# Kernel optimization log

Hardware: AMD Instinct MI355X
Metric: run time of the kernel (lower is better)

## Reference

```python
import jax, jax.numpy as jnp
import numpy as np

ALPHA, BETA, GAMMA = 1.0, 0.5, 0.1
IGNORE = 255


def setup_inputs() -> dict:
    key = jax.random.key(0)
    k1, k2, k3 = jax.random.split(key, 3)
    n, c, h, w, d = 8, 21, 512, 512, 32
    logit = jax.random.normal(k1, (n, c, h, w), dtype=jnp.float32)
    target = jax.random.randint(k2, (n, 1, h, w), 0, 21, dtype=jnp.int32)
    features_in = jax.random.normal(k3, (n, h * w, d), dtype=jnp.float32)
    return {"logit": logit, "target": target, "features_in": features_in}


def reference(logit, target, features_in):
    n, c, h, w = logit.shape
    P = h * w  # total_size per image (sum of all label counts incl. ignore)
    lab = target.reshape(n, P)
    valid = lab != IGNORE
    lab_safe = jnp.where(valid, lab, 0)
    vm = valid.astype(logit.dtype)

    # --- CE loss (mean over non-ignored pixels, as torch CrossEntropyLoss) ---
    logp = jax.nn.log_softmax(logit, axis=1).transpose(0, 2, 3, 1).reshape(n, P, c)
    ce_pix = -jnp.take_along_axis(logp, lab_safe[..., None], axis=2)[..., 0]
    CE = jnp.sum(ce_pix * vm) / jnp.maximum(jnp.sum(vm), 1.0)

    # --- per-pixel logit terms (VAR / Inter), vectorized over the python loop ---
    logit_f = logit.transpose(0, 2, 3, 1).reshape(n, P, c)  # [n,P,c]
    lg = jnp.take_along_axis(logit_f, lab_safe[..., None], axis=2)[..., 0]  # logit at own label
    VAR = jnp.sum(-lg * vm) / P
    Inter = jnp.sum((jnp.sum(logit_f, axis=-1) - lg) * vm) / P

    # --- Center loss: per-image per-class variance of features_in (segment reduce) ---
    onehot = jax.nn.one_hot(lab_safe, c, dtype=logit.dtype) * vm[..., None]  # [n,P,c]
    counts = jnp.sum(onehot, axis=1)                                    # [n,c]
    sums = jnp.einsum('npc,npd->ncd', onehot, features_in)              # class sums
    sumsq = jnp.einsum('npc,np->nc', onehot, jnp.sum(features_in ** 2, axis=-1))
    # sum ||f - mean||^2 = sum||f||^2 - ||sum f||^2 / count
    mean_term = jnp.sum(sums ** 2, axis=-1) / jnp.maximum(counts, 1.0)
    Center = jnp.sum(jnp.where(counts > 0, sumsq - mean_term, 0.0)) / P

    loss = (CE + ALPHA * VAR + BETA * Inter + GAMMA * Center) / n
    return loss
```

## Files before the change

### kernel.cpp

```cpp
#include <hip/hip_runtime.h>


constexpr int   N_IMG  = 8;
constexpr int   C_CLS  = 21;
constexpr int   P_PIX  = 512 * 512;
constexpr int   PQ     = P_PIX / 4;
constexpr int   IGN    = 255;
constexpr float ALPHA  = 1.0f, BETA = 0.5f, GAMMA = 0.1f;

constexpr int MAIN_BLOCKS = 1024;
constexpr int FEAT_ITERS  = 64;

constexpr int OFF_PIX  = 0;
constexpr int OFF_SSQ  = OFF_PIX + MAIN_BLOCKS * 4;
constexpr int OFF_CLS  = OFF_SSQ + MAIN_BLOCKS;
constexpr int OFF_CNT  = OFF_CLS + MAIN_BLOCKS * 672;
constexpr int OFF_MEAN = OFF_CNT + MAIN_BLOCKS * C_CLS;

__global__ __launch_bounds__(256, 4) void main_kernel(
    const float* __restrict__ logit, const int* __restrict__ target,
    const float* __restrict__ feats, float* __restrict__ ws)
{
    __shared__ int    s_hist[C_CLS];
    __shared__ float  s_red[4][4];
    __shared__ float4 s_part[4][8][C_CLS];
    __shared__ float  s_ssq[4];

    const int tid   = threadIdx.x;
    const int img   = blockIdx.x >> 7;
    const int chunk = blockIdx.x & 127;

    if (tid < C_CLS) s_hist[tid] = 0;
    __syncthreads();

    float ce = 0.f, vm = 0.f, var = 0.f, inter = 0.f;

#pragma unroll 1
    for (int qi = 0; qi < 2; ++qi) {
        const int pq = chunk * 512 + qi * 256 + tid;
        const int4 t = ((const int4*)target)[(size_t)img * PQ + pq];
        const float4* lp = (const float4*)logit + (size_t)img * C_CLS * PQ + pq;

        float4 s  = {0.f, 0.f, 0.f, 0.f};
        float4 sc = {0.f, 0.f, 0.f, 0.f};
        float4 lg = {0.f, 0.f, 0.f, 0.f};

#pragma unroll 1
        for (int cb = 0; cb < C_CLS; cb += 7) {
            float4 x[7];
#pragma unroll
            for (int i = 0; i < 7; ++i) x[i] = lp[(size_t)(cb + i) * PQ];
#pragma unroll
            for (int i = 0; i < 7; ++i) {
                const int ch = cb + i;
                const float4 v = x[i];
                s.x += __expf(v.x); s.y += __expf(v.y);
                s.z += __expf(v.z); s.w += __expf(v.w);
                sc.x += v.x; sc.y += v.y; sc.z += v.z; sc.w += v.w;
                lg.x = (t.x == ch) ? v.x : lg.x;
                lg.y = (t.y == ch) ? v.y : lg.y;
                lg.z = (t.z == ch) ? v.z : lg.z;
                lg.w = (t.w == ch) ? v.w : lg.w;
            }
        }

        if (t.x != IGN) atomicAdd(&s_hist[t.x], 1);
        if (t.y != IGN) atomicAdd(&s_hist[t.y], 1);
        if (t.z != IGN) atomicAdd(&s_hist[t.z], 1);
        if (t.w != IGN) atomicAdd(&s_hist[t.w], 1);

        {
            const float v = (t.x != IGN) ? 1.f : 0.f;
            vm += v; ce += v * (__logf(s.x) - lg.x); var -= v * lg.x; inter += v * (sc.x - lg.x);
        }
        {
            const float v = (t.y != IGN) ? 1.f : 0.f;
            vm += v; ce += v * (__logf(s.y) - lg.y); var -= v * lg.y; inter += v * (sc.y - lg.y);
        }
        {
            const float v = (t.z != IGN) ? 1.f : 0.f;
            vm += v; ce += v * (__logf(s.z) - lg.z); var -= v * lg.z; inter += v * (sc.z - lg.z);
        }
        {
            const float v = (t.w != IGN) ? 1.f : 0.f;
            vm += v; ce += v * (__logf(s.w) - lg.w); var -= v * lg.w; inter += v * (sc.w - lg.w);
        }
    }

    for (int off = 32; off; off >>= 1) {
        ce    += __shfl_xor(ce, off);
        vm    += __shfl_xor(vm, off);
        var   += __shfl_xor(var, off);
        inter += __shfl_xor(inter, off);
    }
    const int wv = tid >> 6;
    if ((tid & 63) == 0) {
        s_red[wv][0] = ce; s_red[wv][1] = vm; s_red[wv][2] = var; s_red[wv][3] = inter;
    }
    __syncthreads();

    if (tid < 4) {
        ws[OFF_PIX + blockIdx.x * 4 + tid] =
            s_red[0][tid] + s_red[1][tid] + s_red[2][tid] + s_red[3][tid];
    }
    if (tid < C_CLS) {
        ((int*)ws)[OFF_CNT + blockIdx.x * C_CLS + tid] = s_hist[tid];
    }

    const int p0 = chunk * 2048;
    const int pl = tid >> 3;
    const int dg = tid & 7;

    const float4* fb = (const float4*)feats + ((size_t)img * P_PIX + p0) * 8;
    const int*    tb = target + (size_t)img * P_PIX + p0;

    float4 acc[C_CLS];
#pragma unroll
    for (int c = 0; c < C_CLS; ++c) acc[c] = {0.f, 0.f, 0.f, 0.f};
    float ssq = 0.f;

    int    lab = tb[pl];
    float4 f   = fb[(size_t)pl * 8 + dg];
    for (int it = 0; it < FEAT_ITERS; ++it) {
        int    nlab = 0;
        float4 nf   = {0.f, 0.f, 0.f, 0.f};
        if (it + 1 < FEAT_ITERS) {
            nlab = tb[(it + 1) * 32 + pl];
            nf   = fb[(size_t)((it + 1) * 32 + pl) * 8 + dg];
        }
        const float vld = (lab != IGN) ? 1.f : 0.f;
        ssq += vld * (f.x * f.x + f.y * f.y + f.z * f.z + f.w * f.w);
#pragma unroll
        for (int c = 0; c < C_CLS; ++c) {
            const float m = (lab == c) ? 1.f : 0.f;
            acc[c].x += m * f.x; acc[c].y += m * f.y;
            acc[c].z += m * f.z; acc[c].w += m * f.w;
        }
        lab = nlab; f = nf;
    }

#pragma unroll
    for (int c = 0; c < C_CLS; ++c) {
        for (int off = 8; off <= 32; off <<= 1) {
            acc[c].x += __shfl_xor(acc[c].x, off);
            acc[c].y += __shfl_xor(acc[c].y, off);
            acc[c].z += __shfl_xor(acc[c].z, off);
            acc[c].w += __shfl_xor(acc[c].w, off);
        }
    }
    if ((tid & 63) < 8) {
#pragma unroll
        for (int c = 0; c < C_CLS; ++c) s_part[wv][dg][c] = acc[c];
    }

    for (int off = 1; off < 64; off <<= 1) ssq += __shfl_xor(ssq, off);
    if ((tid & 63) == 0) s_ssq[wv] = ssq;
    __syncthreads();

    if (tid < C_CLS * 8) {
        const int c = tid >> 3, g = tid & 7;
        const float4 a = s_part[0][g][c], b = s_part[1][g][c];
        const float4 d = s_part[2][g][c], e = s_part[3][g][c];
        float4 v;
        v.x = a.x + b.x + d.x + e.x;
        v.y = a.y + b.y + d.y + e.y;
        v.z = a.z + b.z + d.z + e.z;
        v.w = a.w + b.w + d.w + e.w;
        ((float4*)(ws + OFF_CLS))[(size_t)blockIdx.x * 168 + tid] = v;
    }
    if (tid == 0)
        ws[OFF_SSQ + blockIdx.x] = s_ssq[0] + s_ssq[1] + s_ssq[2] + s_ssq[3];
}

__global__ __launch_bounds__(128) void reduce_kernel(float* __restrict__ ws)
{
    __shared__ float sred[128];
    __shared__ int   s_cnt;

    const int img = blockIdx.x / C_CLS;
    const int c   = blockIdx.x % C_CLS;
    const int tid = threadIdx.x;
    const int d   = tid & 31;
    const int qq  = tid >> 5;

    if (tid == 0) s_cnt = 0;
    __syncthreads();

    {
        const int* cp = (const int*)ws + OFF_CNT;
        const int cnt = cp[(img * 128 + tid) * C_CLS + c];
        atomicAdd(&s_cnt, cnt);
    }

    float s = 0.f;
    for (int b = qq; b < 128; b += 4)
        s += ws[OFF_CLS + (size_t)(img * 128 + b) * 672 + c * 32 + d];
    sred[tid] = s;
    __syncthreads();
    if (tid < 64) sred[tid] += sred[tid + 64];
    __syncthreads();
    if (tid < 32) {
        const float Sd = sred[tid] + sred[tid + 32];
        float n2 = Sd * Sd;
        for (int off = 1; off < 32; off <<= 1) n2 += __shfl_xor(n2, off);
        if (tid == 0)
            ws[OFF_MEAN + blockIdx.x] = n2 / fmaxf((float)s_cnt, 1.f);
    }
}

__global__ __launch_bounds__(256) void finalize_kernel(
    const float* __restrict__ ws, float* __restrict__ out)
{
    __shared__ float fr[4][6];
    const int tid = threadIdx.x;

    float ce = 0.f, vm = 0.f, var = 0.f, inter = 0.f, ssq = 0.f, mean = 0.f;
    for (int b = tid; b < MAIN_BLOCKS; b += 256) {
        const float* p = ws + OFF_PIX + b * 4;
        ce += p[0]; vm += p[1]; var += p[2]; inter += p[3];
        ssq += ws[OFF_SSQ + b];
    }
    if (tid < N_IMG * C_CLS) mean = ws[OFF_MEAN + tid];

    for (int off = 32; off; off >>= 1) {
        ce   += __shfl_xor(ce, off);   vm    += __shfl_xor(vm, off);
        var  += __shfl_xor(var, off);  inter += __shfl_xor(inter, off);
        ssq  += __shfl_xor(ssq, off);  mean  += __shfl_xor(mean, off);
    }
    const int wv = tid >> 6;
    if ((tid & 63) == 0) {
        fr[wv][0] = ce;  fr[wv][1] = vm;   fr[wv][2] = var;
        fr[wv][3] = inter; fr[wv][4] = ssq; fr[wv][5] = mean;
    }
    __syncthreads();
    if (tid == 0) {
        const float CE_s  = fr[0][0] + fr[1][0] + fr[2][0] + fr[3][0];
        const float VM    = fr[0][1] + fr[1][1] + fr[2][1] + fr[3][1];
        const float VAR_s = fr[0][2] + fr[1][2] + fr[2][2] + fr[3][2];
        const float INT_s = fr[0][3] + fr[1][3] + fr[2][3] + fr[3][3];
        const float SSQ   = fr[0][4] + fr[1][4] + fr[2][4] + fr[3][4];
        const float MEAN  = fr[0][5] + fr[1][5] + fr[2][5] + fr[3][5];
        const float invP   = 1.f / (float)P_PIX;
        const float CE     = CE_s / fmaxf(VM, 1.f);
        const float VAR    = VAR_s * invP;
        const float Inter  = INT_s * invP;
        const float Center = (SSQ - MEAN) * invP;
        out[0] = (CE + ALPHA * VAR + BETA * Inter + GAMMA * Center) / (float)N_IMG;
    }
}

extern "C" void kernel_launch(void* const* d_in, const int* in_sizes, int n_in,
                              void* d_out, int out_size, void* d_ws, size_t ws_size,
                              hipStream_t stream)
{
    const float* logit  = (const float*)d_in[0];
    const int*   target = (const int*)d_in[1];
    const float* feats  = (const float*)d_in[2];
    float* ws  = (float*)d_ws;
    float* out = (float*)d_out;

    main_kernel    <<<MAIN_BLOCKS, 256, 0, stream>>>(logit, target, feats, ws);
    reduce_kernel  <<<N_IMG * C_CLS, 128, 0, stream>>>(ws);
    finalize_kernel<<<1, 256, 0, stream>>>(ws, out);
}
```

Measured before the change: 507.9 us.

## Stream feature tiles via async global-to-LDS loads with double buffering

The feature pass now copies 64-pixel tiles of the feature array straight into LDS with async global_load_lds, double-buffered so the next tile loads while the current one is accumulated. The first tile is issued before the logit/CE phase so its latency overlaps that work. Labels are staged into LDS during the CE phase and reused, removing the second global read of the target array. The cost is 24KB of LDS per block, which may limit occupancy at 4 blocks per CU, plus extra barriers per tile and reliance on hand-placed vmcnt waits that must match the outstanding load count.

```diff
diff --git a/kernel.cpp b/kernel.cpp
--- a/kernel.cpp
+++ b/kernel.cpp
@@ -9,7 +9,9 @@
 constexpr float ALPHA  = 1.0f, BETA = 0.5f, GAMMA = 0.1f;
 
 constexpr int MAIN_BLOCKS = 1024;
-constexpr int FEAT_ITERS  = 64;
+constexpr int PX_BLK      = 2048;
+constexpr int TILE_PX     = 64;
+constexpr int NT          = PX_BLK / TILE_PX;
 
 constexpr int OFF_PIX  = 0;
 constexpr int OFF_SSQ  = OFF_PIX + MAIN_BLOCKS * 4;
@@ -17,21 +19,40 @@
 constexpr int OFF_CNT  = OFF_CLS + MAIN_BLOCKS * 672;
 constexpr int OFF_MEAN = OFF_CNT + MAIN_BLOCKS * C_CLS;
 
+__device__ __forceinline__ void gl_lds16(const float* g, void* l)
+{
+    __builtin_amdgcn_global_load_lds(
+        (const __attribute__((address_space(1))) void*)g,
+        (__attribute__((address_space(3))) void*)l, 16, 0, 0);
+}
+
 __global__ __launch_bounds__(256, 4) void main_kernel(
     const float* __restrict__ logit, const int* __restrict__ target,
     const float* __restrict__ feats, float* __restrict__ ws)
 {
-    __shared__ int    s_hist[C_CLS];
-    __shared__ float  s_red[4][4];
-    __shared__ float4 s_part[4][8][C_CLS];
-    __shared__ float  s_ssq[4];
+    __shared__ __align__(16) char smem[24 * 1024];
+    __shared__ int   s_hist[C_CLS];
+    __shared__ float s_red[4][4];
+    __shared__ float s_ssq[4];
+
+    int* s_lab = (int*)smem;
 
     const int tid   = threadIdx.x;
     const int img   = blockIdx.x >> 7;
     const int chunk = blockIdx.x & 127;
+    const int p0    = chunk * PX_BLK;
+
+    const float* fbase = feats + ((size_t)img * P_PIX + p0) * 32;
 
     if (tid < C_CLS) s_hist[tid] = 0;
     __syncthreads();
+
+    {
+        gl_lds16(fbase + (size_t)tid * 4,
+                 smem + 8192 + (size_t)(tid & ~63) * 16);
+        gl_lds16(fbase + (size_t)(256 + tid) * 4,
+                 smem + 8192 + (size_t)((256 + tid) & ~63) * 16);
+    }
 
     float ce = 0.f, vm = 0.f, var = 0.f, inter = 0.f;
 
@@ -40,6 +61,8 @@
         const int pq = chunk * 512 + qi * 256 + tid;
         const int4 t = ((const int4*)target)[(size_t)img * PQ + pq];
         const float4* lp = (const float4*)logit + (size_t)img * C_CLS * PQ + pq;
+
+        ((int4*)s_lab)[qi * 256 + tid] = t;
 
         float4 s  = {0.f, 0.f, 0.f, 0.f};
         float4 sc = {0.f, 0.f, 0.f, 0.f};
@@ -107,37 +130,46 @@
         ((int*)ws)[OFF_CNT + blockIdx.x * C_CLS + tid] = s_hist[tid];
     }
 
-    const int p0 = chunk * 2048;
     const int pl = tid >> 3;
     const int dg = tid & 7;
 
-    const float4* fb = (const float4*)feats + ((size_t)img * P_PIX + p0) * 8;
-    const int*    tb = target + (size_t)img * P_PIX + p0;
-
     float4 acc[C_CLS];
 #pragma unroll
     for (int c = 0; c < C_CLS; ++c) acc[c] = {0.f, 0.f, 0.f, 0.f};
     float ssq = 0.f;
 
-    int    lab = tb[pl];
-    float4 f   = fb[(size_t)pl * 8 + dg];
-    for (int it = 0; it < FEAT_ITERS; ++it) {
-        int    nlab = 0;
-        float4 nf   = {0.f, 0.f, 0.f, 0.f};
-        if (it + 1 < FEAT_ITERS) {
-            nlab = tb[(it + 1) * 32 + pl];
-            nf   = fb[(size_t)((it + 1) * 32 + pl) * 8 + dg];
-        }
-        const float vld = (lab != IGN) ? 1.f : 0.f;
-        ssq += vld * (f.x * f.x + f.y * f.y + f.z * f.z + f.w * f.w);
-#pragma unroll
-        for (int c = 0; c < C_CLS; ++c) {
-            const float m = (lab == c) ? 1.f : 0.f;
-            acc[c].x += m * f.x; acc[c].y += m * f.y;
-            acc[c].z += m * f.z; acc[c].w += m * f.w;
-        }
-        lab = nlab; f = nf;
-    }
+#pragma unroll 1
+    for (int tt = 0; tt < NT; ++tt) {
+        const float* cur = (const float*)(smem + 8192 + (size_t)(tt & 1) * 8192);
+        if (tt + 1 < NT) {
+            char* nxt = smem + 8192 + (size_t)((tt + 1) & 1) * 8192;
+            const float* g = fbase + (size_t)(tt + 1) * TILE_PX * 32;
+            gl_lds16(g + (size_t)tid * 4,         nxt + (size_t)(tid & ~63) * 16);
+            gl_lds16(g + (size_t)(256 + tid) * 4, nxt + (size_t)((256 + tid) & ~63) * 16);
+            asm volatile("s_waitcnt vmcnt(2)" ::: "memory");
+        } else {
+            asm volatile("s_waitcnt vmcnt(0)" ::: "memory");
+        }
+        __builtin_amdgcn_s_barrier();
+
+#pragma unroll
+        for (int h = 0; h < 2; ++h) {
+            const int lp2 = h * 32 + pl;
+            const int lab = s_lab[tt * TILE_PX + lp2];
+            const float4 f = ((const float4*)cur)[lp2 * 8 + dg];
+            const float vld = (lab != IGN) ? 1.f : 0.f;
+            ssq += vld * (f.x * f.x + f.y * f.y + f.z * f.z + f.w * f.w);
+#pragma unroll
+            for (int c = 0; c < C_CLS; ++c) {
+                const float m = (lab == c) ? 1.f : 0.f;
+                acc[c].x += m * f.x; acc[c].y += m * f.y;
+                acc[c].z += m * f.z; acc[c].w += m * f.w;
+            }
+        }
+        __builtin_amdgcn_s_barrier();
+    }
+
+    __syncthreads();
 
 #pragma unroll
     for (int c = 0; c < C_CLS; ++c) {
@@ -148,19 +180,22 @@
             acc[c].w += __shfl_xor(acc[c].w, off);
         }
     }
+    for (int off = 1; off < 64; off <<= 1) ssq += __shfl_xor(ssq, off);
+
+    float4* s_part = (float4*)smem;
     if ((tid & 63) < 8) {
 #pragma unroll
-        for (int c = 0; c < C_CLS; ++c) s_part[wv][dg][c] = acc[c];
-    }
-
-    for (int off = 1; off < 64; off <<= 1) ssq += __shfl_xor(ssq, off);
+        for (int c = 0; c < C_CLS; ++c) s_part[(wv * 8 + dg) * C_CLS + c] = acc[c];
+    }
     if ((tid & 63) == 0) s_ssq[wv] = ssq;
     __syncthreads();
 
     if (tid < C_CLS * 8) {
         const int c = tid >> 3, g = tid & 7;
-        const float4 a = s_part[0][g][c], b = s_part[1][g][c];
-        const float4 d = s_part[2][g][c], e = s_part[3][g][c];
+        const float4 a = s_part[(0 * 8 + g) * C_CLS + c];
+        const float4 b = s_part[(1 * 8 + g) * C_CLS + c];
+        const float4 d = s_part[(2 * 8 + g) * C_CLS + c];
+        const float4 e = s_part[(3 * 8 + g) * C_CLS + c];
         float4 v;
         v.x = a.x + b.x + d.x + e.x;
         v.y = a.y + b.y + d.y + e.y;
```

Measured after the change: 511.0 us. No clear change (+0.6%).
